# Kernel optimization log

Measured on AMD Instinct MI355X. Metric: run time of the kernel, lower is better.

Reference implementation:

```python
import jax, jax.numpy as jnp
import numpy as np

NUM_HEADS = 12
HEAD_DIM = 128
DIM = NUM_HEADS * HEAD_DIM  # 1536
FRAMES = 8
GRID_H, GRID_W = 15, 26
SPATIAL = GRID_H * GRID_W  # 390
SEQ = FRAMES * SPATIAL      # 3120
EPS = 1e-5


def setup_inputs() -> dict:
    key = jax.random.key(0)
    ks = jax.random.split(key, 12)
    w = lambda k, shape, s=0.02: jax.random.normal(k, shape, dtype=jnp.float32) * s
    return {
        "x": jax.random.normal(ks[0], (1, SEQ, DIM), dtype=jnp.float32),
        "freqs": jax.random.uniform(ks[1], (SEQ, HEAD_DIM // 2), dtype=jnp.float32) * 6.283,
        "Wq": w(ks[2], (DIM, DIM)), "bq": jnp.zeros((DIM,), jnp.float32), "gq": jnp.ones((DIM,), jnp.float32),
        "Wk": w(ks[3], (DIM, DIM)), "bk": jnp.zeros((DIM,), jnp.float32), "gk": jnp.ones((DIM,), jnp.float32),
        "Wv": w(ks[4], (DIM, DIM)), "bv": jnp.zeros((DIM,), jnp.float32),
        "Wo": w(ks[5], (DIM, DIM)), "bo": jnp.zeros((DIM,), jnp.float32),
        "qk_frame_bias": w(ks[6], (FRAMES, DIM), 0.05),
        "v_frame_bias": w(ks[7], (FRAMES, DIM), 0.05),
        "v_spatial_bias": w(ks[8], (SPATIAL, DIM), 0.05),
    }


def _rmsnorm(x, g):
    return x * jax.lax.rsqrt(jnp.mean(x * x, axis=-1, keepdims=True) + EPS) * g


def _rope(x, freqs):
    # x: [b, s, dim] -> per-head interleaved complex rotation (Wan-style)
    b, s, _ = x.shape
    xp = x.reshape(b, s, NUM_HEADS, HEAD_DIM // 2, 2)
    cos = jnp.cos(freqs)[None, :, None, :]  # [1, s, 1, d/2]
    sin = jnp.sin(freqs)[None, :, None, :]
    xr, xi = xp[..., 0], xp[..., 1]
    out = jnp.stack([xr * cos - xi * sin, xr * sin + xi * cos], axis=-1)
    return out.reshape(b, s, DIM)


def _expand_frame(bias):
    # [FRAMES, dim] -> [1, FRAMES*SPATIAL, dim] (each frame vector repeated over spatial tokens)
    return jnp.broadcast_to(bias[:, None, :], (FRAMES, SPATIAL, DIM)).reshape(1, SEQ, DIM)


def _expand_spatial(bias):
    # [SPATIAL, dim] -> [1, FRAMES*SPATIAL, dim] (tiled over frames)
    return jnp.broadcast_to(bias[None, :, :], (FRAMES, SPATIAL, DIM)).reshape(1, SEQ, DIM)


def reference(x, freqs, Wq, bq, gq, Wk, bk, gk, Wv, bv, Wo, bo,
              qk_frame_bias, v_frame_bias, v_spatial_bias):
    q = _rmsnorm(x @ Wq + bq, gq)
    k = _rmsnorm(x @ Wk + bk, gk)
    v = x @ Wv + bv
    q = _rope(q, freqs)
    k = _rope(k, freqs)
    qk_bias = _expand_frame(qk_frame_bias)
    q = q + qk_bias
    k = k + qk_bias
    v = v + _expand_frame(v_frame_bias) + _expand_spatial(v_spatial_bias)
    b, s, _ = x.shape
    qh = q.reshape(b, s, NUM_HEADS, HEAD_DIM)
    kh = k.reshape(b, s, NUM_HEADS, HEAD_DIM)
    vh = v.reshape(b, s, NUM_HEADS, HEAD_DIM)
    scale = 1.0 / np.sqrt(HEAD_DIM)
    scores = jnp.einsum("bqnd,bknd->bnqk", qh, kh) * scale
    attn = jax.nn.softmax(scores, axis=-1)
    out = jnp.einsum("bnqk,bknd->bqnd", attn, vh).reshape(b, s, DIM)
    return out @ Wo + bo
```

## Files before the change

### kernel.cpp

```cpp
#include <hip/hip_runtime.h>
#include <cstdint>

#define SEQ     3120
#define SPAD    3200
#define DIM     1536
#define NQKV    4608
#define HEADS   12
#define HD      128
#define SPATIAL 390
#define EPSV    1e-5f
#define KVBLK   64
#define NTILES  49
#define NEGBIG  (-1e30f)
#define QSCALE  (0.08838834764831845f * 1.4426950408889634f)
#define CROW(r, hi) ((((r) & 3) + 8 * ((r) >> 2)) + 4 * (hi))

typedef unsigned short u16;
typedef short s16x8 __attribute__((ext_vector_type(8)));
typedef float f32x4 __attribute__((ext_vector_type(4)));
typedef float f32x16 __attribute__((ext_vector_type(16)));

__device__ __forceinline__ u16 f2bf(float f) {
  union { float f; unsigned u; } v; v.f = f;
  unsigned r = v.u + 0x7FFFu + ((v.u >> 16) & 1u);
  return (u16)(r >> 16);
}
__device__ __forceinline__ float bf2f(u16 b) {
  union { unsigned u; float f; } v; v.u = ((unsigned)b) << 16;
  return v.f;
}
__device__ __forceinline__ unsigned cvtpk(float lo, float hi) {
  unsigned r;
  asm("v_cvt_pk_bf16_f32 %0, %1, %2" : "=v"(r) : "v"(lo), "v"(hi));
  return r;
}
__device__ __forceinline__ void gload16(const void* g, const void* l) {
  __builtin_amdgcn_global_load_lds(
      (const __attribute__((address_space(1))) unsigned*)g,
      (__attribute__((address_space(3))) unsigned*)(uintptr_t)l,
      16, 0, 0);
}

__global__ __launch_bounds__(256) void k_convert_x(
    const float* __restrict__ x, const float* __restrict__ bq,
    const float* __restrict__ bk, const float* __restrict__ bv,
    u16* __restrict__ xb, float* __restrict__ bcat) {
  if (blockIdx.x == 0) {
    for (int j = threadIdx.x; j < NQKV; j += 256)
      bcat[j] = (j < DIM) ? bq[j] : (j < 2 * DIM) ? bk[j - DIM] : bv[j - 2 * DIM];
  }
  const int i = (blockIdx.x * 256 + threadIdx.x) * 4;
  if (i >= SPAD * DIM) return;
  const int row = i / DIM;
  float4 v = make_float4(0.f, 0.f, 0.f, 0.f);
  if (row < SEQ) v = *(const float4*)(x + i);
  const unsigned lo = (unsigned)f2bf(v.x) | ((unsigned)f2bf(v.y) << 16);
  const unsigned hi = (unsigned)f2bf(v.z) | ((unsigned)f2bf(v.w) << 16);
  *(uint2*)(xb + i) = make_uint2(lo, hi);
}

__global__ __launch_bounds__(256) void k_transpose_w(
    const float* __restrict__ Wq, const float* __restrict__ Wk,
    const float* __restrict__ Wv, const float* __restrict__ Wo,
    u16* __restrict__ WtAll, u16* __restrict__ WoT) {
  const int wsel = blockIdx.z;
  const float* W = (wsel == 0) ? Wq : (wsel == 1) ? Wk : (wsel == 2) ? Wv : Wo;
  __shared__ float t[32][33];
  const int k0 = blockIdx.x * 32, n0 = blockIdx.y * 32;
  const int c = threadIdx.x & 31, r8 = threadIdx.x >> 5;
#pragma unroll
  for (int rr = 0; rr < 32; rr += 8)
    t[r8 + rr][c] = W[(size_t)(k0 + r8 + rr) * DIM + n0 + c];
  __syncthreads();
  u16* Wt = (wsel < 3) ? (WtAll + (size_t)wsel * DIM * DIM) : WoT;
#pragma unroll
  for (int rr = 0; rr < 32; rr += 8)
    Wt[(size_t)(n0 + r8 + rr) * DIM + k0 + c] = f2bf(t[c][r8 + rr]);
}

template <int OUT_BF16>
__global__ __launch_bounds__(256) void k_gemm(const u16* __restrict__ A,
                                              const u16* __restrict__ Bt,
                                              const float* __restrict__ bias,
                                              void* __restrict__ Cout,
                                              int N, int K, int storeMmax,
                                              int nbx) {
  __shared__ short As[8192];
  __shared__ short Bs[8192];
  const int nwg = gridDim.x;
  const int q = nwg >> 3, r = nwg & 7;
  const int xcd = blockIdx.x & 7, idx = blockIdx.x >> 3;
  const int swz = (xcd < r ? xcd * (q + 1) : r * (q + 1) + (xcd - r) * q) + idx;
  const int bxi = swz % nbx, byi = swz / nbx;
  const int brow = byi * 128, bcol = bxi * 128;

  const int tid = threadIdx.x;
  const int lane = tid & 63, wv = tid >> 6;
  const int l15 = lane & 15, g = lane >> 4;
  const int wr = wv >> 1, wc = wv & 1;

  const f32x4 z4 = {0.f, 0.f, 0.f, 0.f};
  f32x4 acc[4][4];
#pragma unroll
  for (int m = 0; m < 4; ++m)
#pragma unroll
    for (int n = 0; n < 4; ++n) acc[m][n] = z4;

  const u16* Ap[4];
  const u16* Bp[4];
  const int sch = ((lane & 7) ^ ((lane >> 3) & 7)) * 8;
#pragma unroll
  for (int it = 0; it < 4; ++it) {
    const int row = it * 32 + wv * 8 + (lane >> 3);
    Ap[it] = A + (size_t)(brow + row) * K + sch;
    Bp[it] = Bt + (size_t)(bcol + row) * K + sch;
  }

  for (int k0 = 0; k0 < K; k0 += 64) {
    __syncthreads();
#pragma unroll
    for (int it = 0; it < 4; ++it) {
      gload16(Ap[it] + k0, As + (it * 32 + wv * 8) * 64);
      gload16(Bp[it] + k0, Bs + (it * 32 + wv * 8) * 64);
    }
    __syncthreads();
#pragma unroll
    for (int kk = 0; kk < 2; ++kk) {
      s16x8 a[4], b[4];
#pragma unroll
      for (int m = 0; m < 4; ++m)
        a[m] = *(const s16x8*)&As[(wr * 64 + m * 16 + l15) * 64 +
                                  (((kk * 4 + g) ^ (l15 & 7)) * 8)];
#pragma unroll
      for (int n = 0; n < 4; ++n)
        b[n] = *(const s16x8*)&Bs[(wc * 64 + n * 16 + l15) * 64 +
                                  (((kk * 4 + g) ^ (l15 & 7)) * 8)];
#pragma unroll
      for (int m = 0; m < 4; ++m)
#pragma unroll
        for (int n = 0; n < 4; ++n)
          acc[m][n] = __builtin_amdgcn_mfma_f32_16x16x32_bf16(a[m], b[n], acc[m][n], 0, 0, 0);
    }
  }

#pragma unroll
  for (int m = 0; m < 4; ++m) {
#pragma unroll
    for (int n = 0; n < 4; ++n) {
      const int cc = bcol + wc * 64 + n * 16 + l15;
      const float bb = bias[cc];
#pragma unroll
      for (int i = 0; i < 4; ++i) {
        const int rr = brow + wr * 64 + m * 16 + g * 4 + i;
        if (rr < storeMmax) {
          const float v = acc[m][n][i] + bb;
          if (OUT_BF16) ((u16*)Cout)[(size_t)rr * N + cc] = f2bf(v);
          else          ((float*)Cout)[(size_t)rr * N + cc] = v;
        }
      }
    }
  }
}

__global__ __launch_bounds__(256) void k_post(
    const u16* __restrict__ Pqkv, const float* __restrict__ freqs,
    const float* __restrict__ gq, const float* __restrict__ gk,
    const float* __restrict__ qkfb, const float* __restrict__ vfb,
    const float* __restrict__ vsb,
    u16* __restrict__ Qf, u16* __restrict__ Kf, u16* __restrict__ Vf) {
  const int s = blockIdx.x;
  const int t = threadIdx.x;
  const int fidx = s / SPATIAL;
  const int sp = s - fidx * SPATIAL;
  __shared__ float cs[64], sn[64];
  __shared__ float red[8];
  if (t < 64) {
    const float a = freqs[s * 64 + t];
    cs[t] = __cosf(a);
    sn[t] = __sinf(a);
  }
  const u16* qrow = Pqkv + (size_t)s * NQKV;
  const u16* krow = qrow + DIM;
  const u16* vrow = qrow + 2 * DIM;
  float sq = 0.f, sk = 0.f;
  for (int i = t; i < DIM; i += 256) {
    const float a = bf2f(qrow[i]); sq += a * a;
    const float b = bf2f(krow[i]); sk += b * b;
  }
#pragma unroll
  for (int off = 1; off < 64; off <<= 1) {
    sq += __shfl_xor(sq, off);
    sk += __shfl_xor(sk, off);
  }
  const int lane = t & 63, wv = t >> 6;
  if (lane == 0) { red[wv] = sq; red[wv + 4] = sk; }
  __syncthreads();
  sq = red[0] + red[1] + red[2] + red[3];
  sk = red[4] + red[5] + red[6] + red[7];
  const float rq = rsqrtf(sq * (1.0f / DIM) + EPSV);
  const float rk = rsqrtf(sk * (1.0f / DIM) + EPSV);
  for (int p = t; p < 768; p += 256) {
    const int d = 2 * p;
    const int pin = p & 63;
    const float c = cs[pin], s_ = sn[pin];
    const float bq0 = qkfb[fidx * DIM + d], bq1 = qkfb[fidx * DIM + d + 1];
    float xr = bf2f(qrow[d]) * rq * gq[d];
    float xi = bf2f(qrow[d + 1]) * rq * gq[d + 1];
    const float q0 = (xr * c - xi * s_ + bq0) * QSCALE;
    const float q1 = (xr * s_ + xi * c + bq1) * QSCALE;
    *(unsigned*)&Qf[(size_t)s * DIM + d] = (unsigned)f2bf(q0) | ((unsigned)f2bf(q1) << 16);
    xr = bf2f(krow[d]) * rk * gk[d];
    xi = bf2f(krow[d + 1]) * rk * gk[d + 1];
    const float k0 = xr * c - xi * s_ + bq0;
    const float k1 = xr * s_ + xi * c + bq1;
    *(unsigned*)&Kf[(size_t)s * DIM + d] = (unsigned)f2bf(k0) | ((unsigned)f2bf(k1) << 16);
    const float v0 = bf2f(vrow[d]) + vfb[fidx * DIM + d] + vsb[(size_t)sp * DIM + d];
    const float v1 = bf2f(vrow[d + 1]) + vfb[fidx * DIM + d + 1] + vsb[(size_t)sp * DIM + d + 1];
    *(unsigned*)&Vf[(size_t)s * DIM + d] = (unsigned)f2bf(v0) | ((unsigned)f2bf(v1) << 16);
  }
}

__global__ __launch_bounds__(256) void k_transpose_v(const u16* __restrict__ Vf,
                                                     u16* __restrict__ Vt) {
  __shared__ u16 tile[64][65];
  const int s0 = blockIdx.x * 64, c0 = blockIdx.y * 64;
  const int c = threadIdx.x & 63, r4 = threadIdx.x >> 6;
#pragma unroll
  for (int rr = 0; rr < 64; rr += 4) {
    const int s = s0 + r4 + rr;
    tile[r4 + rr][c] = (s < SEQ) ? Vf[(size_t)s * DIM + c0 + c] : (u16)0;
  }
  __syncthreads();
#pragma unroll
  for (int rr = 0; rr < 64; rr += 4) {
    const int dglob = c0 + r4 + rr;
    Vt[(size_t)dglob * SPAD + s0 + c] = tile[c][r4 + rr];
  }
}

__global__ __launch_bounds__(320, 2) void k_attn(const u16* __restrict__ Qf,
                                                 const u16* __restrict__ Kf,
                                                 const u16* __restrict__ Vt,
                                                 u16* __restrict__ AttO) {
  __shared__ short Ks[2][8192];
  __shared__ short Vs[2][8192];
  const int h = blockIdx.y;
  const int tid = threadIdx.x;
  const int lane = tid & 63, w = tid >> 6;
  const int l31 = lane & 31, hi = lane >> 5;
  const int qrow = blockIdx.x * 160 + w * 32 + l31;

  s16x8 qb[8];
  {
    const u16* qp = Qf + (size_t)qrow * DIM + h * HD + hi * 8;
#pragma unroll
    for (int s = 0; s < 8; ++s) qb[s] = *(const s16x8*)(qp + s * 16);
  }

  f32x16 o[4];
#pragma unroll
  for (int d = 0; d < 4; ++d)
#pragma unroll
    for (int r = 0; r < 16; ++r) o[d][r] = 0.f;
  float sl = 0.f;

  const u16* Kp[4];
  const u16* Vp[4];
  if (w < 4) {
#pragma unroll
    for (int it = 0; it < 4; ++it) {
      const int krow = w * 16 + it * 4 + (lane >> 4);
      const int kch = (lane & 15) ^ (it * 4 + (lane >> 4));
      Kp[it] = Kf + (size_t)krow * DIM + h * HD + kch * 8;
      const int vrow = w * 32 + it * 8 + (lane >> 3);
      const int vch = (lane & 7) ^ (lane >> 3);
      Vp[it] = Vt + (size_t)(h * HD + vrow) * SPAD + vch * 8;
    }
  }
  auto stage = [&](int T, int B) {
    const size_t kof = (size_t)T * KVBLK * DIM;
    const int vof = T * KVBLK;
#pragma unroll
    for (int it = 0; it < 4; ++it) {
      gload16(Kp[it] + kof, &Ks[B][(w * 16 + it * 4) * 128]);
      gload16(Vp[it] + vof, &Vs[B][(w * 32 + it * 8) * 64]);
    }
  };

  if (w < 4) {
    asm volatile("s_waitcnt vmcnt(0)" ::: "memory");
    stage(0, 0);
  }

  for (int t = 0; t < NTILES; ++t) {
    const int b = t & 1;
    if (w < 4) {
      if (t + 1 < NTILES) {
        stage(t + 1, b ^ 1);
        asm volatile("s_waitcnt vmcnt(8)" ::: "memory");
      } else {
        asm volatile("s_waitcnt vmcnt(0)" ::: "memory");
      }
    }
    __builtin_amdgcn_s_barrier();
    __builtin_amdgcn_sched_barrier(0);

    f32x16 st[2];
#pragma unroll
    for (int r = 0; r < 16; ++r) { st[0][r] = 0.f; st[1][r] = 0.f; }
    __builtin_amdgcn_s_setprio(1);
#pragma unroll
    for (int grp = 0; grp < 2; ++grp)
#pragma unroll
      for (int s = 0; s < 8; ++s) {
        const s16x8 ka = *(const s16x8*)&Ks[b][(grp * 32 + l31) * 128 +
                                              (((2 * s + hi) ^ (lane & 15)) * 8)];
        st[grp] = __builtin_amdgcn_mfma_f32_32x32x16_bf16(ka, qb[s], st[grp], 0, 0, 0);
      }
    __builtin_amdgcn_s_setprio(0);

    s16x8 vb[4][4];
#pragma unroll
    for (int s = 0; s < 4; ++s)
#pragma unroll
      for (int d = 0; d < 4; ++d)
        vb[s][d] = *(const s16x8*)&Vs[b][(d * 32 + l31) * 64 +
                                         (((2 * s + hi) ^ (lane & 7)) * 8)];

    if (t == NTILES - 1) {
#pragma unroll
      for (int r = 8; r < 16; ++r) st[1][r] = NEGBIG;
    }
    unsigned W[16], X[16];
    float p0s = 0.f, p1s = 0.f, p2s = 0.f, p3s = 0.f;
#pragma unroll
    for (int grp = 0; grp < 2; ++grp)
#pragma unroll
      for (int i = 0; i < 8; ++i) {
        const float p0 = exp2f(st[grp][2 * i]);
        const float p1 = exp2f(st[grp][2 * i + 1]);
        if (grp) { p2s += p0; p3s += p1; } else { p0s += p0; p1s += p1; }
        W[grp * 8 + i] = cvtpk(p0, p1);
      }
    sl += (p0s + p1s) + (p2s + p3s);
#pragma unroll
    for (int j = 0; j < 16; ++j) X[j] = __shfl_xor((int)W[j], 32);

    __builtin_amdgcn_s_setprio(1);
#pragma unroll
    for (int s = 0; s < 4; ++s) {
      const int base = (s >> 1) * 8 + (s & 1) * 4;
      unsigned pw[4];
      pw[0] = hi ? X[base + 2] : W[base + 0];
      pw[1] = hi ? X[base + 3] : W[base + 1];
      pw[2] = hi ? W[base + 2] : X[base + 0];
      pw[3] = hi ? W[base + 3] : X[base + 1];
      const s16x8 pa = *(const s16x8*)pw;
#pragma unroll
      for (int d = 0; d < 4; ++d)
        o[d] = __builtin_amdgcn_mfma_f32_32x32x16_bf16(pa, vb[s][d], o[d], 0, 0, 0);
    }
    __builtin_amdgcn_s_setprio(0);
    __builtin_amdgcn_s_barrier();
    __builtin_amdgcn_sched_barrier(0);
  }

  sl += __shfl_xor(sl, 32);
  const float rs = 1.0f / sl;
#pragma unroll
  for (int r = 0; r < 16; ++r) {
    const float rq = __shfl(rs, CROW(r, hi));
    const int row = blockIdx.x * 160 + w * 32 + CROW(r, hi);
    if (row < SEQ) {
#pragma unroll
      for (int d = 0; d < 4; ++d)
        AttO[(size_t)row * DIM + h * HD + d * 32 + l31] = f2bf(o[d][r] * rq);
    }
  }
}

extern "C" void kernel_launch(void* const* d_in, const int* in_sizes, int n_in,
                              void* d_out, int out_size, void* d_ws, size_t ws_size,
                              hipStream_t stream) {
  const float* x    = (const float*)d_in[0];
  const float* freqs= (const float*)d_in[1];
  const float* Wq   = (const float*)d_in[2];
  const float* bq   = (const float*)d_in[3];
  const float* gq   = (const float*)d_in[4];
  const float* Wk   = (const float*)d_in[5];
  const float* bk   = (const float*)d_in[6];
  const float* gk   = (const float*)d_in[7];
  const float* Wv   = (const float*)d_in[8];
  const float* bv   = (const float*)d_in[9];
  const float* Wo   = (const float*)d_in[10];
  const float* bo   = (const float*)d_in[11];
  const float* qkfb = (const float*)d_in[12];
  const float* vfb  = (const float*)d_in[13];
  const float* vsb  = (const float*)d_in[14];

  if (ws_size < (size_t)87705600) return;

  char* ws = (char*)d_ws;
  u16*   xb    = (u16*)(ws);
  u16*   Vt    = (u16*)(ws);
  u16*   WtAll = (u16*)(ws + 9830400);
  u16*   WoT   = (u16*)(ws + 23986176);
  float* bcat  = (float*)(ws + 28704768);
  u16*   Pqkv  = (u16*)(ws + 28723200);
  u16*   AttO  = (u16*)(ws + 28723200);
  u16*   Qf    = (u16*)(ws + 58214400);
  u16*   Kf    = (u16*)(ws + 68044800);
  u16*   Vf    = (u16*)(ws + 77875200);

  k_convert_x<<<4800, 256, 0, stream>>>(x, bq, bk, bv, xb, bcat);
  k_transpose_w<<<dim3(48, 48, 4), 256, 0, stream>>>(Wq, Wk, Wv, Wo, WtAll, WoT);
  k_gemm<1><<<900, 256, 0, stream>>>(xb, WtAll, bcat, Pqkv, NQKV, DIM, SPAD, 36);
  k_post<<<SEQ, 256, 0, stream>>>(Pqkv, freqs, gq, gk, qkfb, vfb, vsb, Qf, Kf, Vf);
  k_transpose_v<<<dim3(50, 24), 256, 0, stream>>>(Vf, Vt);
  k_attn<<<dim3(20, 12), 320, 0, stream>>>(Qf, Kf, Vt, AttO);
  k_gemm<0><<<300, 256, 0, stream>>>(AttO, WoT, bo, d_out, DIM, DIM, SEQ, 12);
}
```

Measured before the change: 259.5 us.

## Vectorize post-processing, widen weight transpose tiles, and XCD-remap attention blocks

```diff
diff --git a/kernel.cpp b/kernel.cpp
--- a/kernel.cpp
+++ b/kernel.cpp
@@ -65,17 +65,23 @@
     u16* __restrict__ WtAll, u16* __restrict__ WoT) {
   const int wsel = blockIdx.z;
   const float* W = (wsel == 0) ? Wq : (wsel == 1) ? Wk : (wsel == 2) ? Wv : Wo;
-  __shared__ float t[32][33];
-  const int k0 = blockIdx.x * 32, n0 = blockIdx.y * 32;
-  const int c = threadIdx.x & 31, r8 = threadIdx.x >> 5;
-#pragma unroll
-  for (int rr = 0; rr < 32; rr += 8)
-    t[r8 + rr][c] = W[(size_t)(k0 + r8 + rr) * DIM + n0 + c];
+  __shared__ float t[64][65];
+  const int k0 = blockIdx.x * 64, n0 = blockIdx.y * 64;
+  const int c = threadIdx.x & 63, r4 = threadIdx.x >> 6;
+#pragma unroll
+  for (int rr = 0; rr < 64; rr += 4)
+    t[r4 + rr][c] = W[(size_t)(k0 + r4 + rr) * DIM + n0 + c];
   __syncthreads();
   u16* Wt = (wsel < 3) ? (WtAll + (size_t)wsel * DIM * DIM) : WoT;
-#pragma unroll
-  for (int rr = 0; rr < 32; rr += 8)
-    Wt[(size_t)(n0 + r8 + rr) * DIM + k0 + c] = f2bf(t[c][r8 + rr]);
+  const int kp = threadIdx.x & 31;
+  const int r8 = threadIdx.x >> 5;
+#pragma unroll
+  for (int rr = 0; rr < 64; rr += 8) {
+    const int n = r8 + rr;
+    const unsigned v = (unsigned)f2bf(t[2 * kp][n]) |
+                       ((unsigned)f2bf(t[2 * kp + 1][n]) << 16);
+    *(unsigned*)&Wt[(size_t)(n0 + n) * DIM + k0 + 2 * kp] = v;
+  }
 }
 
 template <int OUT_BF16>
@@ -182,10 +188,17 @@
   const u16* qrow = Pqkv + (size_t)s * NQKV;
   const u16* krow = qrow + DIM;
   const u16* vrow = qrow + 2 * DIM;
+  s16x8 q8, k8, v8;
   float sq = 0.f, sk = 0.f;
-  for (int i = t; i < DIM; i += 256) {
-    const float a = bf2f(qrow[i]); sq += a * a;
-    const float b = bf2f(krow[i]); sk += b * b;
+  if (t < 192) {
+    q8 = *(const s16x8*)(qrow + 8 * t);
+    k8 = *(const s16x8*)(krow + 8 * t);
+    v8 = *(const s16x8*)(vrow + 8 * t);
+#pragma unroll
+    for (int i = 0; i < 8; ++i) {
+      const float a = bf2f((u16)q8[i]); sq += a * a;
+      const float b = bf2f((u16)k8[i]); sk += b * b;
+    }
   }
 #pragma unroll
   for (int off = 1; off < 64; off <<= 1) {
@@ -199,25 +212,41 @@
   sk = red[4] + red[5] + red[6] + red[7];
   const float rq = rsqrtf(sq * (1.0f / DIM) + EPSV);
   const float rk = rsqrtf(sk * (1.0f / DIM) + EPSV);
-  for (int p = t; p < 768; p += 256) {
-    const int d = 2 * p;
-    const int pin = p & 63;
+  if (t >= 192) return;
+  const int d0 = 8 * t;
+  float GQ[8], GK[8], FB[8], VF[8], VS[8];
+  *(float4*)&GQ[0] = *(const float4*)(gq + d0);
+  *(float4*)&GQ[4] = *(const float4*)(gq + d0 + 4);
+  *(float4*)&GK[0] = *(const float4*)(gk + d0);
+  *(float4*)&GK[4] = *(const float4*)(gk + d0 + 4);
+  *(float4*)&FB[0] = *(const float4*)(qkfb + fidx * DIM + d0);
+  *(float4*)&FB[4] = *(const float4*)(qkfb + fidx * DIM + d0 + 4);
+  *(float4*)&VF[0] = *(const float4*)(vfb + fidx * DIM + d0);
+  *(float4*)&VF[4] = *(const float4*)(vfb + fidx * DIM + d0 + 4);
+  *(float4*)&VS[0] = *(const float4*)(vsb + (size_t)sp * DIM + d0);
+  *(float4*)&VS[4] = *(const float4*)(vsb + (size_t)sp * DIM + d0 + 4);
+  unsigned qo[4], ko[4], vo[4];
+#pragma unroll
+  for (int pi = 0; pi < 4; ++pi) {
+    const int pin = (4 * t + pi) & 63;
     const float c = cs[pin], s_ = sn[pin];
-    const float bq0 = qkfb[fidx * DIM + d], bq1 = qkfb[fidx * DIM + d + 1];
-    float xr = bf2f(qrow[d]) * rq * gq[d];
-    float xi = bf2f(qrow[d + 1]) * rq * gq[d + 1];
-    const float q0 = (xr * c - xi * s_ + bq0) * QSCALE;
-    const float q1 = (xr * s_ + xi * c + bq1) * QSCALE;
-    *(unsigned*)&Qf[(size_t)s * DIM + d] = (unsigned)f2bf(q0) | ((unsigned)f2bf(q1) << 16);
-    xr = bf2f(krow[d]) * rk * gk[d];
-    xi = bf2f(krow[d + 1]) * rk * gk[d + 1];
-    const float k0 = xr * c - xi * s_ + bq0;
-    const float k1 = xr * s_ + xi * c + bq1;
-    *(unsigned*)&Kf[(size_t)s * DIM + d] = (unsigned)f2bf(k0) | ((unsigned)f2bf(k1) << 16);
-    const float v0 = bf2f(vrow[d]) + vfb[fidx * DIM + d] + vsb[(size_t)sp * DIM + d];
-    const float v1 = bf2f(vrow[d + 1]) + vfb[fidx * DIM + d + 1] + vsb[(size_t)sp * DIM + d + 1];
-    *(unsigned*)&Vf[(size_t)s * DIM + d] = (unsigned)f2bf(v0) | ((unsigned)f2bf(v1) << 16);
-  }
+    float xr = bf2f((u16)q8[2 * pi]) * rq * GQ[2 * pi];
+    float xi = bf2f((u16)q8[2 * pi + 1]) * rq * GQ[2 * pi + 1];
+    const float q0 = (xr * c - xi * s_ + FB[2 * pi]) * QSCALE;
+    const float q1 = (xr * s_ + xi * c + FB[2 * pi + 1]) * QSCALE;
+    qo[pi] = (unsigned)f2bf(q0) | ((unsigned)f2bf(q1) << 16);
+    xr = bf2f((u16)k8[2 * pi]) * rk * GK[2 * pi];
+    xi = bf2f((u16)k8[2 * pi + 1]) * rk * GK[2 * pi + 1];
+    const float kk0 = xr * c - xi * s_ + FB[2 * pi];
+    const float kk1 = xr * s_ + xi * c + FB[2 * pi + 1];
+    ko[pi] = (unsigned)f2bf(kk0) | ((unsigned)f2bf(kk1) << 16);
+    const float v0 = bf2f((u16)v8[2 * pi]) + VF[2 * pi] + VS[2 * pi];
+    const float v1 = bf2f((u16)v8[2 * pi + 1]) + VF[2 * pi + 1] + VS[2 * pi + 1];
+    vo[pi] = (unsigned)f2bf(v0) | ((unsigned)f2bf(v1) << 16);
+  }
+  *(uint4*)(Qf + (size_t)s * DIM + d0) = make_uint4(qo[0], qo[1], qo[2], qo[3]);
+  *(uint4*)(Kf + (size_t)s * DIM + d0) = make_uint4(ko[0], ko[1], ko[2], ko[3]);
+  *(uint4*)(Vf + (size_t)s * DIM + d0) = make_uint4(vo[0], vo[1], vo[2], vo[3]);
 }
 
 __global__ __launch_bounds__(256) void k_transpose_v(const u16* __restrict__ Vf,
@@ -244,11 +273,14 @@
                                                  u16* __restrict__ AttO) {
   __shared__ short Ks[2][8192];
   __shared__ short Vs[2][8192];
-  const int h = blockIdx.y;
+  const int bid = blockIdx.x;
+  const int gb = (bid & 7) * 30 + (bid >> 3);
+  const int h = gb / 20;
+  const int bx = gb - h * 20;
   const int tid = threadIdx.x;
   const int lane = tid & 63, w = tid >> 6;
   const int l31 = lane & 31, hi = lane >> 5;
-  const int qrow = blockIdx.x * 160 + w * 32 + l31;
+  const int qrow = bx * 160 + w * 32 + l31;
 
   s16x8 qb[8];
   {
@@ -370,7 +402,7 @@
 #pragma unroll
   for (int r = 0; r < 16; ++r) {
     const float rq = __shfl(rs, CROW(r, hi));
-    const int row = blockIdx.x * 160 + w * 32 + CROW(r, hi);
+    const int row = bx * 160 + w * 32 + CROW(r, hi);
     if (row < SEQ) {
 #pragma unroll
       for (int d = 0; d < 4; ++d)
@@ -413,10 +445,10 @@
   u16*   Vf    = (u16*)(ws + 77875200);
 
   k_convert_x<<<4800, 256, 0, stream>>>(x, bq, bk, bv, xb, bcat);
-  k_transpose_w<<<dim3(48, 48, 4), 256, 0, stream>>>(Wq, Wk, Wv, Wo, WtAll, WoT);
+  k_transpose_w<<<dim3(24, 24, 4), 256, 0, stream>>>(Wq, Wk, Wv, Wo, WtAll, WoT);
   k_gemm<1><<<900, 256, 0, stream>>>(xb, WtAll, bcat, Pqkv, NQKV, DIM, SPAD, 36);
   k_post<<<SEQ, 256, 0, stream>>>(Pqkv, freqs, gq, gk, qkfb, vfb, vsb, Qf, Kf, Vf);
   k_transpose_v<<<dim3(50, 24), 256, 0, stream>>>(Vf, Vt);
-  k_attn<<<dim3(20, 12), 320, 0, stream>>>(Qf, Kf, Vt, AttO);
+  k_attn<<<240, 320, 0, stream>>>(Qf, Kf, Vt, AttO);
   k_gemm<0><<<300, 256, 0, stream>>>(AttO, WoT, bo, d_out, DIM, DIM, SEQ, 12);
 }
```

After: 255.2 us. Within noise of the previous version (-1.6%).
